# Kernel optimization log

Hardware: AMD Instinct MI355X
Metric: run time of the kernel (lower is better)

## Reference

```python
import jax, jax.numpy as jnp
import numpy as np

L, D, H, FF = 4, 512, 8, 2048
B, S = 32, 512
DK = D // H
EPS = 1e-5


def setup_inputs() -> dict:
    key = jax.random.key(0)
    ks = iter(jax.random.split(key, 20))
    r = lambda *sh: 0.02 * jax.random.normal(next(ks), sh, dtype=jnp.float32)
    inp = {
        "src": jax.random.normal(next(ks), (B, S, D), dtype=jnp.float32),
        "Wq": r(L, D, D), "bq": jnp.zeros((L, D), jnp.float32),
        "Wk": r(L, D, D), "bk": jnp.zeros((L, D), jnp.float32),
        "Wv": r(L, D, D), "bv": jnp.zeros((L, D), jnp.float32),
        "Wo": r(L, D, D), "bo": jnp.zeros((L, D), jnp.float32),
        "ln1_g": jnp.ones((L, D), jnp.float32), "ln1_b": jnp.zeros((L, D), jnp.float32),
        "ln2_g": jnp.ones((L, D), jnp.float32), "ln2_b": jnp.zeros((L, D), jnp.float32),
        "Wf1": r(L, D, FF), "bf1": jnp.zeros((L, FF), jnp.float32),
        "Wf2": r(L, FF, D), "bf2": jnp.zeros((L, D), jnp.float32),
    }
    return inp


def _ln(x, g, b):
    m = jnp.mean(x, -1, keepdims=True)
    v = jnp.mean(jnp.square(x - m), -1, keepdims=True)
    return (x - m) * jax.lax.rsqrt(v + EPS) * g + b


def reference(src, Wq, bq, Wk, bk, Wv, bv, Wo, bo,
              ln1_g, ln1_b, ln2_g, ln2_b, Wf1, bf1, Wf2, bf2):
    b, s, d = src.shape
    scale = DK ** -0.5
    x = src
    scores = None  # residual attention: raw pre-softmax scores carried across layers
    for i in range(L):
        q = (jnp.einsum('bsd,de->bse', x, Wq[i]) + bq[i]).reshape(b, s, H, DK)
        k = (jnp.einsum('bsd,de->bse', x, Wk[i]) + bk[i]).reshape(b, s, H, DK)
        v = (jnp.einsum('bsd,de->bse', x, Wv[i]) + bv[i]).reshape(b, s, H, DK)
        attn_scores = jnp.einsum('bqhd,bkhd->bhqk', q, k) * scale  # [B,H,S,S]
        if scores is not None:
            attn_scores = attn_scores + scores
        scores = attn_scores
        w = jax.nn.softmax(attn_scores, axis=-1)
        o = jnp.einsum('bhqk,bkhd->bqhd', w, v).reshape(b, s, d)
        o = jnp.einsum('bsd,de->bse', o, Wo[i]) + bo[i]
        x = _ln(x + o, ln1_g[i], ln1_b[i])  # post-norm
        h = jax.nn.gelu(jnp.einsum('bsd,df->bsf', x, Wf1[i]) + bf1[i], approximate=False)
        ff = jnp.einsum('bsf,fd->bsd', h, Wf2[i]) + bf2[i]
        x = _ln(x + ff, ln2_g[i], ln2_b[i])
    return x
```

## Files before the change

kernel.cpp:

```cpp
#include <hip/hip_runtime.h>
#include <hip/hip_bf16.h>


#define NL 4
#define DMODEL 512
#define NH 8
#define FFDIM 2048
#define BATCH 32
#define SEQ 512
#define DHEAD 64
#define NTOK (BATCH*SEQ)
#define LDQKV (3*DMODEL)

typedef unsigned short u16;
typedef __bf16 bf16x8 __attribute__((ext_vector_type(8)));
typedef float f32x4 __attribute__((ext_vector_type(4)));
typedef unsigned short u16x8 __attribute__((ext_vector_type(8)));
typedef unsigned short u16x4 __attribute__((ext_vector_type(4)));

__device__ __forceinline__ u16 f2b(float f){
  unsigned u = __builtin_bit_cast(unsigned, f);
  return (u16)((u + 0x7FFFu + ((u>>16)&1u)) >> 16);
}
__device__ __forceinline__ float b2f(u16 h){
  return __builtin_bit_cast(float, ((unsigned)h)<<16);
}
__device__ __forceinline__ void gll16(const void* g, void* l){
  __builtin_amdgcn_global_load_lds((__attribute__((address_space(1))) void*)(g),
                                   (__attribute__((address_space(3))) void*)(l), 16, 0, 0);
}
__device__ __forceinline__ float wred_sum(float v){
  #pragma unroll
  for (int off=32; off; off>>=1) v += __shfl_xor(v, off, 64);
  return v;
}
__device__ __forceinline__ float gelu_f(float v){
  float y = 0.79788456080286536f*(v + 0.044715f*v*v*v);
  float t = __expf(2.0f*y);
  return v - v/(t + 1.0f);
}

template<int OUT_MODE>
__global__ __launch_bounds__(256) void gemm_bt(
    const u16* __restrict__ A, const u16* __restrict__ Bt,
    const float* __restrict__ bias, u16* __restrict__ Cout,
    int M, int N, int K)
{
  __shared__ u16 smem[16384];
  const int t = threadIdx.x;
  const int w = t>>6, lane = t&63;

  const int gx = gridDim.x;
  const int id = blockIdx.y*gx + blockIdx.x;
  const int cpx = (gx*gridDim.y) >> 3;
  const int nid = (id & 7)*cpx + (id >> 3);
  const int m0 = (nid / gx)*128, n0 = (nid % gx)*128;

  const int wr = (w>>1)*64, wc = (w&1)*64;

  f32x4 acc[4][4];
  #pragma unroll
  for (int m=0;m<4;m++)
    #pragma unroll
    for (int n=0;n<4;n++) acc[m][n] = f32x4{0.f,0.f,0.f,0.f};

  const int srow = t>>2;
  const int scol = (((t&3) ^ ((srow>>1)&3)))*8;
  const size_t aBase = (size_t)(m0 + srow)*K + scol;
  const size_t bBase = (size_t)(n0 + srow)*K + scol;
  const size_t rstep = (size_t)64*K;
  const int dstw = w*512;

  #define STAGE(buf, k0) do{                                       \
    u16* base_ = smem + (buf)*8192;                                \
    gll16(A  + aBase + (k0),          base_ + dstw);               \
    gll16(A  + aBase + rstep + (k0),  base_ + 2048 + dstw);        \
    gll16(Bt + bBase + (k0),          base_ + 4096 + dstw);        \
    gll16(Bt + bBase + rstep + (k0),  base_ + 6144 + dstw);        \
  }while(0)

  const int g = lane>>4, r16 = lane&15;
  const int chunkoff = ((g ^ ((r16>>1)&3))<<3);

  STAGE(0, 0);
  int cur = 0;
  for (int k0=0; k0<K; k0+=32){
    if (k0+32 < K){
      STAGE(cur^1, k0+32);
      asm volatile("s_waitcnt vmcnt(4)" ::: "memory");
    } else {
      asm volatile("s_waitcnt vmcnt(0)" ::: "memory");
    }
    asm volatile("s_barrier" ::: "memory");
    const u16* lA = smem + cur*8192;
    const u16* lB = lA + 4096;
    bf16x8 af[4], bfr[4];
    #pragma unroll
    for (int m=0;m<4;m++) af[m]  = *(const bf16x8*)(lA + (wr+m*16+r16)*32 + chunkoff);
    #pragma unroll
    for (int n=0;n<4;n++) bfr[n] = *(const bf16x8*)(lB + (wc+n*16+r16)*32 + chunkoff);
    #pragma unroll
    for (int m=0;m<4;m++)
      #pragma unroll
      for (int n=0;n<4;n++)
        acc[m][n] = __builtin_amdgcn_mfma_f32_16x16x32_bf16(af[m], bfr[n], acc[m][n], 0,0,0);
    asm volatile("s_waitcnt lgkmcnt(0)" ::: "memory");
    asm volatile("s_barrier" ::: "memory");
    cur ^= 1;
  }
  #undef STAGE

  const int c16 = lane&15, r4 = (lane>>4)*4;
  float bb[4];
  #pragma unroll
  for (int n=0;n<4;n++) bb[n] = bias[n0 + wc + n*16 + c16];
  #pragma unroll
  for (int s=0;s<2;s++){
    __syncthreads();
    if ((w>>1)==s){
      #pragma unroll
      for (int m=0;m<4;m++)
        #pragma unroll
        for (int n=0;n<4;n++)
          #pragma unroll
          for (int j=0;j<4;j++){
            float val = acc[m][n][j] + bb[n];
            if (OUT_MODE==2) val = gelu_f(val);
            const int row = m*16 + r4 + j;
            const int col = (wc + n*16 + c16) ^ (((row>>2)&3)<<4);
            smem[row*128 + col] = f2b(val);
          }
    }
    __syncthreads();
    #pragma unroll
    for (int i=0;i<4;i++){
      const int lrow = i*16 + (t>>4), colr = (t&15)*8;
      u16x8 vv = *(const u16x8*)(smem + lrow*128 + (colr ^ (((lrow>>2)&3)<<4)));
      *(u16x8*)(Cout + (size_t)(m0 + s*64 + lrow)*N + n0 + colr) = vv;
    }
  }
}

__global__ __launch_bounds__(256) void transpose_v(
    const u16* __restrict__ qkv, u16* __restrict__ vt)
{
  __shared__ u16 T[64*33];
  const int t = threadIdx.x;
  const int s0 = blockIdx.x*32;
  const int bh = blockIdx.y;
  const int b = bh >> 3, h = bh & 7;
  const u16* v = qkv + 2*DMODEL + h*DHEAD;
  #pragma unroll
  for (int i=0;i<8;i++){
    int idx = i*256 + t;
    int sl = idx >> 6, d = idx & 63;
    T[d*33 + sl] = v[(size_t)(b*SEQ + s0 + sl)*LDQKV + d];
  }
  __syncthreads();
  u16* o = vt + (size_t)bh*DHEAD*SEQ;
  #pragma unroll
  for (int i=0;i<8;i++){
    int idx = i*256 + t;
    int d = idx >> 5, sl = idx & 31;
    o[(size_t)d*SEQ + s0 + sl] = T[d*33 + sl];
  }
}

template<int ADDP, int WRITES>
__global__ __launch_bounds__(256) void fused_attn(
    const u16* __restrict__ qkv, const u16* __restrict__ vt,
    u16* __restrict__ sc, u16* __restrict__ outp)
{
  __shared__ u16 smem[20480];
  u16* lQ = smem;
  const int t=threadIdx.x, w=t>>6, lane=t&63;
  const int g = lane>>4, r16 = lane&15;

  const int dd = blockIdx.x;
  const int c  = dd&7;
  const int j_ = dd>>3;
  const int qb = j_&7;
  const int bh = (j_>>3)*8 + c;
  const int b = bh>>3, h = bh&7;
  const int q0 = qb*64;

  const int srow = t>>3;
  const int schunk = (t&7) ^ (srow&7);
  const u16* qp = qkv + h*DHEAD;
  const u16* kp = qkv + DMODEL + h*DHEAD;
  const size_t qBase = (size_t)(b*SEQ + q0 + srow)*LDQKV + (size_t)(schunk*8);
  const size_t kRow0 = (size_t)(b*SEQ + srow)*LDQKV + (size_t)(schunk*8);

  #pragma unroll
  for (int r=0;r<2;r++)
    gll16(qp + qBase + (size_t)(r*32)*LDQKV, lQ + r*2048 + w*512);
  #pragma unroll
  for (int r=0;r<4;r++)
    gll16(kp + kRow0 + (size_t)(r*32)*LDQKV, smem + 4096 + r*2048 + w*512);
  __syncthreads();

  u16* srowp = sc + (size_t)bh*SEQ*SEQ;
  const u16* vtp = vt + (size_t)bh*DHEAD*SEQ;

  bf16x8 ones;
  #pragma unroll
  for (int j=0;j<8;j++) ones[j] = (__bf16)1.0f;

  f32x4 pvacc[4][4], rs[4];
  #pragma unroll
  for (int nf=0;nf<4;nf++){
    rs[nf] = f32x4{0.f,0.f,0.f,0.f};
    #pragma unroll
    for (int nd=0;nd<4;nd++) pvacc[nf][nd] = f32x4{0.f,0.f,0.f,0.f};
  }

  #pragma unroll
  for (int kt=0; kt<4; kt++){
    const int cur = 4096 + (kt&1)*8192;
    const int nxt = 4096 + ((kt+1)&1)*8192;
    const int ktw = kt*128 + w*32;

    u16x4 sold[2][4];
    if (ADDP){
      #pragma unroll
      for (int mf=0;mf<2;mf++)
        #pragma unroll
        for (int nf=0;nf<4;nf++)
          sold[mf][nf] = *(const u16x4*)(srowp + (size_t)(q0+nf*16+r16)*SEQ + ktw + mf*16 + g*4);
    }

    f32x4 acc[2][4];
    #pragma unroll
    for (int mf=0;mf<2;mf++)
      #pragma unroll
      for (int nf=0;nf<4;nf++) acc[mf][nf] = f32x4{0.f,0.f,0.f,0.f};
    #pragma unroll
    for (int ks=0; ks<2; ks++){
      bf16x8 af[2], bfq[4];
      #pragma unroll
      for (int mf=0;mf<2;mf++){
        const int row = w*32 + mf*16 + r16;
        af[mf] = *(const bf16x8*)(smem + cur + row*64 + (((ks*4+g)^(row&7))<<3));
      }
      #pragma unroll
      for (int nf=0;nf<4;nf++){
        const int row = nf*16 + r16;
        bfq[nf] = *(const bf16x8*)(lQ + row*64 + (((ks*4+g)^(row&7))<<3));
      }
      #pragma unroll
      for (int mf=0;mf<2;mf++)
        #pragma unroll
        for (int nf=0;nf<4;nf++)
          acc[mf][nf] = __builtin_amdgcn_mfma_f32_16x16x32_bf16(af[mf], bfq[nf], acc[mf][nf], 0,0,0);
    }

    if (kt<3){
      const size_t kB = kRow0 + (size_t)((kt+1)*128)*LDQKV;
      #pragma unroll
      for (int r=0;r<4;r++)
        gll16(kp + kB + (size_t)(r*32)*LDQKV, smem + nxt + r*2048 + w*512);
    }

    bf16x8 pe[4];
    #pragma unroll
    for (int nf=0;nf<4;nf++){
      u16x8 pk;
      #pragma unroll
      for (int mf=0;mf<2;mf++){
        float v[4]; u16x4 sn;
        #pragma unroll
        for (int j=0;j<4;j++){
          v[j] = acc[mf][nf][j]*0.125f;
          if (ADDP) v[j] += b2f(sold[mf][nf][j]);
          if (WRITES) sn[j] = f2b(v[j]);
          pk[mf*4+j] = f2b(__expf(v[j]));
        }
        if (WRITES)
          *(u16x4*)(srowp + (size_t)(q0+nf*16+r16)*SEQ + ktw + mf*16 + g*4) = sn;
      }
      pe[nf] = __builtin_bit_cast(bf16x8, pk);
      rs[nf] = __builtin_amdgcn_mfma_f32_16x16x32_bf16(pe[nf], ones, rs[nf], 0,0,0);
    }

    #pragma unroll
    for (int nd=0;nd<4;nd++){
      const u16* vr = vtp + (size_t)(nd*16+r16)*SEQ + ktw + g*4;
      u16x4 v0 = *(const u16x4*)(vr);
      u16x4 v1 = *(const u16x4*)(vr + 16);
      u16x8 vv;
      #pragma unroll
      for (int j=0;j<4;j++){ vv[j] = v0[j]; vv[4+j] = v1[j]; }
      bf16x8 vb = __builtin_bit_cast(bf16x8, vv);
      #pragma unroll
      for (int nf=0;nf<4;nf++)
        pvacc[nf][nd] = __builtin_amdgcn_mfma_f32_16x16x32_bf16(pe[nf], vb, pvacc[nf][nd], 0,0,0);
    }

    __syncthreads();
  }

  float* bufO = (float*)smem;
  float* bufR = ((float*)smem) + 4096;
  if (r16 == 0){
    #pragma unroll
    for (int nf=0;nf<4;nf++)
      #pragma unroll
      for (int j=0;j<4;j++)
        bufR[w*64 + nf*16 + g*4 + j] = rs[nf][j];
  }
  if (w == 0){
    #pragma unroll
    for (int nf=0;nf<4;nf++)
      #pragma unroll
      for (int nd=0;nd<4;nd++)
        #pragma unroll
        for (int j=0;j<4;j++)
          bufO[(nf*16+g*4+j)*64 + nd*16+r16] = pvacc[nf][nd][j];
  }
  __syncthreads();
  #pragma unroll
  for (int ww=1; ww<4; ww++){
    if (w == ww){
      #pragma unroll
      for (int nf=0;nf<4;nf++)
        #pragma unroll
        for (int nd=0;nd<4;nd++)
          #pragma unroll
          for (int j=0;j<4;j++)
            bufO[(nf*16+g*4+j)*64 + nd*16+r16] += pvacc[nf][nd][j];
    }
    __syncthreads();
  }
  {
    const int q = t>>2, db = (t&3)*16;
    const float tot = bufR[q] + bufR[64+q] + bufR[128+q] + bufR[192+q];
    const float inv = 1.0f/tot;
    u16* ob = outp + ((size_t)(b*SEQ + q0 + q)*NH + h)*DHEAD + db;
    u16x8 o0, o1;
    #pragma unroll
    for (int j=0;j<8;j++) o0[j] = f2b(bufO[q*64 + db + j]*inv);
    #pragma unroll
    for (int j=0;j<8;j++) o1[j] = f2b(bufO[q*64 + db + 8 + j]*inv);
    *(u16x8*)(ob)     = o0;
    *(u16x8*)(ob + 8) = o1;
  }
}

template<int WF>
__global__ __launch_bounds__(256) void ln_k(
    const u16* __restrict__ xin, const u16* __restrict__ proj,
    const float* __restrict__ g, const float* __restrict__ beta,
    u16* __restrict__ xb, float* __restrict__ fout)
{
  const int row = blockIdx.x*4 + (threadIdx.x>>6);
  const int lane = threadIdx.x & 63;
  const size_t base = (size_t)row*DMODEL + lane*8;
  u16x8 a = *(const u16x8*)(xin + base);
  u16x8 p = *(const u16x8*)(proj + base);
  float v[8];
  #pragma unroll
  for (int j=0;j<8;j++) v[j] = b2f(a[j]) + b2f(p[j]);
  float s = 0.f;
  #pragma unroll
  for (int j=0;j<8;j++) s += v[j];
  s = wred_sum(s);
  const float mean = s * (1.0f/DMODEL);
  float qv = 0.f;
  #pragma unroll
  for (int j=0;j<8;j++){ float d = v[j]-mean; qv += d*d; }
  qv = wred_sum(qv);
  const float rstd = rsqrtf(qv*(1.0f/DMODEL) + 1e-5f);
  const int c = lane*8;
  float o[8]; u16x8 ob;
  #pragma unroll
  for (int j=0;j<8;j++){
    o[j] = (v[j]-mean)*rstd*g[c+j] + beta[c+j];
    ob[j] = f2b(o[j]);
  }
  *(u16x8*)(xb + base) = ob;
  if (WF){
    *(float4*)(fout + base)     = make_float4(o[0],o[1],o[2],o[3]);
    *(float4*)(fout + base + 4) = make_float4(o[4],o[5],o[6],o[7]);
  }
}

__global__ __launch_bounds__(256) void wt_conv(
    const float* __restrict__ Win, u16* __restrict__ Wout,
    int K, int N, long outLstride)
{
  __shared__ float T[32][33];
  const int t = threadIdx.x;
  const int tx = t&31, ty = t>>5;
  const int n0 = blockIdx.x*32, k0 = blockIdx.y*32, l = blockIdx.z;
  const float* W = Win + (size_t)l*K*N;
  u16* O = Wout + (size_t)l*outLstride;
  #pragma unroll
  for (int i=0;i<4;i++)
    T[ty+i*8][tx] = W[(size_t)(k0+ty+i*8)*N + n0 + tx];
  __syncthreads();
  #pragma unroll
  for (int i=0;i<4;i++){
    const int nn = ty + i*8;
    O[(size_t)(n0+nn)*K + k0 + tx] = f2b(T[tx][nn]);
  }
}

__global__ void bias_concat(const float* __restrict__ bq, const float* __restrict__ bk,
                            const float* __restrict__ bv, float* __restrict__ out)
{
  const int i = blockIdx.x*256 + threadIdx.x;
  if (i >= NL*LDQKV) return;
  const int l = i / LDQKV, c = i % LDQKV;
  float v;
  if (c < DMODEL)        v = bq[l*DMODEL + c];
  else if (c < 2*DMODEL) v = bk[l*DMODEL + c - DMODEL];
  else                   v = bv[l*DMODEL + c - 2*DMODEL];
  out[i] = v;
}

__global__ void conv_src(const float* __restrict__ src, u16* __restrict__ xb)
{
  const int i = blockIdx.x*256 + threadIdx.x;
  float4 v = ((const float4*)src)[i];
  u16x4 bb; bb[0]=f2b(v.x); bb[1]=f2b(v.y); bb[2]=f2b(v.z); bb[3]=f2b(v.w);
  *(u16x4*)(xb + (size_t)i*4) = bb;
}

__global__ void diag_fill(float* __restrict__ o, int n, float v){
  int i = blockIdx.x*256 + threadIdx.x;
  if (i < n) o[i] = v;
}

extern "C" void kernel_launch(void* const* d_in, const int* in_sizes, int n_in,
                              void* d_out, int out_size, void* d_ws, size_t ws_size,
                              hipStream_t stream)
{
  (void)in_sizes; (void)n_in;
  const float* src = (const float*)d_in[0];
  const float* Wq  = (const float*)d_in[1];
  const float* bq  = (const float*)d_in[2];
  const float* Wk  = (const float*)d_in[3];
  const float* bk  = (const float*)d_in[4];
  const float* Wv  = (const float*)d_in[5];
  const float* bv  = (const float*)d_in[6];
  const float* Wo  = (const float*)d_in[7];
  const float* bo  = (const float*)d_in[8];
  const float* ln1g= (const float*)d_in[9];
  const float* ln1b= (const float*)d_in[10];
  const float* ln2g= (const float*)d_in[11];
  const float* ln2b= (const float*)d_in[12];
  const float* Wf1 = (const float*)d_in[13];
  const float* bf1 = (const float*)d_in[14];
  const float* Wf2 = (const float*)d_in[15];
  const float* bf2 = (const float*)d_in[16];

  const size_t NEEDED = 260071424ull;
  if (ws_size < NEEDED){
    diag_fill<<<(out_size+255)/256, 256, 0, stream>>>((float*)d_out, out_size,
                                                      (float)(ws_size >> 20));
    return;
  }
  char* ws = (char*)d_ws;
  u16*  xb     = (u16*)(ws + 0);
  u16*  qkv    = (u16*)(ws + 16777216);
  u16*  attn_o = (u16*)(ws + 16777216);
  u16*  hbuf   = (u16*)(ws + 16777216);
  u16*  vt     = (u16*)(ws + 67108864);
  u16*  scores = (u16*)(ws + 83886080);
  u16*  proj   = (u16*)(ws + 218103808);
  u16*  wqkvT  = (u16*)(ws + 234881024);
  u16*  woT    = (u16*)(ws + 241172480);
  u16*  wf1T   = (u16*)(ws + 243269632);
  u16*  wf2T   = (u16*)(ws + 251658240);
  float* qkvb  = (float*)(ws + 260046848);

  dim3 blk(256);

  wt_conv<<<dim3(16,16,4),blk,0,stream>>>(Wq, wqkvT,                  DMODEL, DMODEL, (long)LDQKV*DMODEL);
  wt_conv<<<dim3(16,16,4),blk,0,stream>>>(Wk, wqkvT + DMODEL*DMODEL,  DMODEL, DMODEL, (long)LDQKV*DMODEL);
  wt_conv<<<dim3(16,16,4),blk,0,stream>>>(Wv, wqkvT + 2*DMODEL*DMODEL,DMODEL, DMODEL, (long)LDQKV*DMODEL);
  wt_conv<<<dim3(16,16,4),blk,0,stream>>>(Wo, woT,  DMODEL, DMODEL, (long)DMODEL*DMODEL);
  wt_conv<<<dim3(64,16,4),blk,0,stream>>>(Wf1, wf1T, DMODEL, FFDIM, (long)FFDIM*DMODEL);
  wt_conv<<<dim3(16,64,4),blk,0,stream>>>(Wf2, wf2T, FFDIM, DMODEL, (long)DMODEL*FFDIM);
  bias_concat<<<24,blk,0,stream>>>(bq,bk,bv,qkvb);
  conv_src<<<8192,blk,0,stream>>>(src, xb);

  for (int l=0; l<NL; l++){
    gemm_bt<0><<<dim3(12,128),blk,0,stream>>>(xb, wqkvT + (size_t)l*LDQKV*DMODEL,
                                              qkvb + l*LDQKV, qkv, NTOK, LDQKV, DMODEL);
    transpose_v<<<dim3(16,BATCH*NH),blk,0,stream>>>(qkv, vt);
    if (l==0)
      fused_attn<0,1><<<dim3(2048),blk,0,stream>>>(qkv, vt, scores, attn_o);
    else if (l<NL-1)
      fused_attn<1,1><<<dim3(2048),blk,0,stream>>>(qkv, vt, scores, attn_o);
    else
      fused_attn<1,0><<<dim3(2048),blk,0,stream>>>(qkv, vt, scores, attn_o);
    gemm_bt<0><<<dim3(4,128),blk,0,stream>>>(attn_o, woT + (size_t)l*DMODEL*DMODEL,
                                             bo + l*DMODEL, proj, NTOK, DMODEL, DMODEL);
    ln_k<0><<<NTOK/4,blk,0,stream>>>(xb, proj, ln1g + l*DMODEL, ln1b + l*DMODEL, xb, nullptr);
    gemm_bt<2><<<dim3(16,128),blk,0,stream>>>(xb, wf1T + (size_t)l*FFDIM*DMODEL,
                                              bf1 + l*FFDIM, hbuf, NTOK, FFDIM, DMODEL);
    gemm_bt<0><<<dim3(4,128),blk,0,stream>>>(hbuf, wf2T + (size_t)l*DMODEL*FFDIM,
                                             bf2 + l*DMODEL, proj, NTOK, DMODEL, FFDIM);
    if (l==NL-1)
      ln_k<1><<<NTOK/4,blk,0,stream>>>(xb, proj, ln2g + l*DMODEL, ln2b + l*DMODEL, xb, (float*)d_out);
    else
      ln_k<0><<<NTOK/4,blk,0,stream>>>(xb, proj, ln2g + l*DMODEL, ln2b + l*DMODEL, xb, nullptr);
  }
}
```

Before: 1.185 ms.

## Store residual scores in fragment-native blocked layout and parallelize PV reduction

The carried pre-softmax score buffer is now stored in a per-(head, q-block, k-tile, wave, lane) blocked layout, so each lane's old-score reads and new-score writes are contiguous 8-byte accesses forming coalesced 2KB blocks instead of strided row accesses. The cross-wave reduction of the PV accumulators now uses two padded LDS buffers (row stride 68) written in parallel by pairs of waves, which cuts the serialized barrier chain and bank conflicts. This relies on every producer and consumer of the score buffer agreeing on the new layout; the buffer is private to this kernel across layers.

```diff
diff --git a/kernel.cpp b/kernel.cpp
--- a/kernel.cpp
+++ b/kernel.cpp
@@ -199,7 +199,7 @@
     gll16(kp + kRow0 + (size_t)(r*32)*LDQKV, smem + 4096 + r*2048 + w*512);
   __syncthreads();
 
-  u16* srowp = sc + (size_t)bh*SEQ*SEQ;
+  u16* sblk = sc + ((((size_t)bh*8 + qb)*4)*4 + w)*2048 + lane*4;
   const u16* vtp = vt + (size_t)bh*DHEAD*SEQ;
 
   bf16x8 ones;
@@ -219,6 +219,7 @@
     const int cur = 4096 + (kt&1)*8192;
     const int nxt = 4096 + ((kt+1)&1)*8192;
     const int ktw = kt*128 + w*32;
+    u16* skt = sblk + (size_t)kt*16384;
 
     u16x4 sold[2][4];
     if (ADDP){
@@ -226,7 +227,7 @@
       for (int mf=0;mf<2;mf++)
         #pragma unroll
         for (int nf=0;nf<4;nf++)
-          sold[mf][nf] = *(const u16x4*)(srowp + (size_t)(q0+nf*16+r16)*SEQ + ktw + mf*16 + g*4);
+          sold[mf][nf] = *(const u16x4*)(skt + (mf*4+nf)*256);
     }
 
     f32x4 acc[2][4];
@@ -276,7 +277,7 @@
           pk[mf*4+j] = f2b(__expf(v[j]));
         }
         if (WRITES)
-          *(u16x4*)(srowp + (size_t)(q0+nf*16+r16)*SEQ + ktw + mf*16 + g*4) = sn;
+          *(u16x4*)(skt + (mf*4+nf)*256) = sn;
       }
       pe[nf] = __builtin_bit_cast(bf16x8, pk);
       rs[nf] = __builtin_amdgcn_mfma_f32_16x16x32_bf16(pe[nf], ones, rs[nf], 0,0,0);
@@ -299,8 +300,9 @@
     __syncthreads();
   }
 
-  float* bufO = (float*)smem;
-  float* bufR = ((float*)smem) + 4096;
+  float* bufA = (float*)smem;
+  float* bufB = bufA + 64*68;
+  float* bufR = bufB + 64*68;
   if (r16 == 0){
     #pragma unroll
     for (int nf=0;nf<4;nf++)
@@ -308,39 +310,40 @@
       for (int j=0;j<4;j++)
         bufR[w*64 + nf*16 + g*4 + j] = rs[nf][j];
   }
-  if (w == 0){
+  if (w < 2){
+    float* dst = (w==0) ? bufA : bufB;
     #pragma unroll
     for (int nf=0;nf<4;nf++)
       #pragma unroll
       for (int nd=0;nd<4;nd++)
         #pragma unroll
         for (int j=0;j<4;j++)
-          bufO[(nf*16+g*4+j)*64 + nd*16+r16] = pvacc[nf][nd][j];
+          dst[(nf*16+g*4+j)*68 + nd*16+r16] = pvacc[nf][nd][j];
   }
   __syncthreads();
-  #pragma unroll
-  for (int ww=1; ww<4; ww++){
-    if (w == ww){
-      #pragma unroll
-      for (int nf=0;nf<4;nf++)
+  if (w >= 2){
+    float* dst = (w==2) ? bufA : bufB;
+    #pragma unroll
+    for (int nf=0;nf<4;nf++)
+      #pragma unroll
+      for (int nd=0;nd<4;nd++)
         #pragma unroll
-        for (int nd=0;nd<4;nd++)
-          #pragma unroll
-          for (int j=0;j<4;j++)
-            bufO[(nf*16+g*4+j)*64 + nd*16+r16] += pvacc[nf][nd][j];
-    }
-    __syncthreads();
-  }
+        for (int j=0;j<4;j++)
+          dst[(nf*16+g*4+j)*68 + nd*16+r16] += pvacc[nf][nd][j];
+  }
+  __syncthreads();
   {
     const int q = t>>2, db = (t&3)*16;
     const float tot = bufR[q] + bufR[64+q] + bufR[128+q] + bufR[192+q];
     const float inv = 1.0f/tot;
+    const float* ra = bufA + q*68 + db;
+    const float* rb = bufB + q*68 + db;
     u16* ob = outp + ((size_t)(b*SEQ + q0 + q)*NH + h)*DHEAD + db;
     u16x8 o0, o1;
     #pragma unroll
-    for (int j=0;j<8;j++) o0[j] = f2b(bufO[q*64 + db + j]*inv);
-    #pragma unroll
-    for (int j=0;j<8;j++) o1[j] = f2b(bufO[q*64 + db + 8 + j]*inv);
+    for (int j=0;j<8;j++) o0[j] = f2b((ra[j]   + rb[j]  )*inv);
+    #pragma unroll
+    for (int j=0;j<8;j++) o1[j] = f2b((ra[8+j] + rb[8+j])*inv);
     *(u16x8*)(ob)     = o0;
     *(u16x8*)(ob + 8) = o1;
   }
```

Result: faster. 1.092 ms (-7.8%).
